# Performance work log

Hardware: AMD Instinct MI355X
Metric: run time of the kernel (lower is better)

## Reference

```python
import jax, jax.numpy as jnp
import numpy as np

VOCAB = 100000
DIM = 300
N, P, D = 4096, 10, 17  # samples, paths per sample (2C), padded path depth


def setup_inputs() -> dict:
    key = jax.random.key(0)
    k1, k2, k3, k4, k5 = jax.random.split(key, 5)
    word_idx = jax.random.randint(k1, (N,), 0, VOCAB)
    paths = jax.random.randint(k2, (N, P, D), 0, VOCAB - 1)   # inner-node ids
    labels = jax.random.randint(k3, (N, P, D), 0, 2)          # branch directions
    emb1 = jax.random.normal(k4, (VOCAB, DIM), dtype=jnp.float32) * 0.1
    emb2 = jax.random.normal(k5, (VOCAB - 1, DIM), dtype=jnp.float32) * 0.1
    return {"word_idx": word_idx, "paths": paths, "labels": labels,
            "emb1": emb1, "emb2": emb2}


def reference(word_idx, paths, labels, emb1, emb2):
    # proj = embedding_1(x_idx): [N, DIM]
    proj = emb1[word_idx]
    # hierarchy_vectors = embedding_2(dir_path): [N, P, D, DIM]
    hvecs = emb2[paths]
    # output = sigmoid(proj @ hvecs.T), batched over (N, P): [N, P, D]
    logits = jnp.einsum('nd,npkd->npk', proj, hvecs)
    output = jax.nn.sigmoid(logits)
    # mask[output >= 0.5] = 1; target[mask == label] = 1
    mask = (output >= 0.5).astype(labels.dtype)
    target = (mask == labels).astype(jnp.float32)
    return output, target
```

## Files before the change

### kernel.cpp

```cpp
#include <hip/hip_runtime.h>
#include <math.h>

#define NN 4096
#define PP 10
#define DD 17
#define DIM 300
#define NPD (NN * PP * DD)

__global__ __launch_bounds__(256) void hs_fwd_kernel(
    const int* __restrict__ word_idx,
    const int* __restrict__ paths,
    const int* __restrict__ labels,
    const float* __restrict__ emb1,
    const float* __restrict__ emb2,
    float* __restrict__ out,
    float* __restrict__ target)
{
    const int wave = (int)((blockIdx.x * blockDim.x + threadIdx.x) >> 6);
    const int lane = (int)(threadIdx.x & 63);
    if (wave >= NN * PP) return;
    const int n = wave / PP;
    const int j    = lane & 31;
    const int half = lane >> 5;

    const float4* p4 = (const float4*)(emb1 + (long long)word_idx[n] * DIM);
    const float4 pr0 = p4[j];
    const float4 pr1 = p4[j + 32];
    const float4 pr2 = (j < 11) ? p4[j + 64] : make_float4(0.f, 0.f, 0.f, 0.f);

    const long long base = (long long)wave * DD;
    const int my_path  = (lane < DD) ? paths[base + lane]  : 0;
    const int my_label = (lane < DD) ? labels[base + lane] : 0;

    float my_logit = 0.0f;

    #pragma unroll
    for (int i = 0; i < 9; ++i) {
        const int k = 2 * i + half;
        float acc = 0.0f;
        if (k < DD) {
            const int row = __shfl(my_path, k);
            const float4* r4 = (const float4*)(emb2 + (long long)row * DIM);
            const float4 a0 = r4[j];
            const float4 a1 = r4[j + 32];
            acc = pr0.x * a0.x + pr0.y * a0.y + pr0.z * a0.z + pr0.w * a0.w
                + pr1.x * a1.x + pr1.y * a1.y + pr1.z * a1.z + pr1.w * a1.w;
            if (j < 11) {
                const float4 a2 = r4[j + 64];
                acc += pr2.x * a2.x + pr2.y * a2.y + pr2.z * a2.z + pr2.w * a2.w;
            }
        }
        #pragma unroll
        for (int off = 16; off > 0; off >>= 1)
            acc += __shfl_xor(acc, off);
        const float other = __shfl_xor(acc, 32);
        if (lane == 2 * i) my_logit = acc;
        if (2 * i + 1 < DD && lane == 2 * i + 1) my_logit = other;
    }

    if (lane < DD) {
        const float o = 1.0f / (1.0f + expf(-my_logit));
        out[base + lane] = o;
        const int mask = (o >= 0.5f) ? 1 : 0;
        target[base + lane] = (mask == my_label) ? 1.0f : 0.0f;
    }
}

extern "C" void kernel_launch(void* const* d_in, const int* in_sizes, int n_in,
                              void* d_out, int out_size, void* d_ws, size_t ws_size,
                              hipStream_t stream) {
    const int*   word_idx = (const int*)d_in[0];
    const int*   paths    = (const int*)d_in[1];
    const int*   labels   = (const int*)d_in[2];
    const float* emb1     = (const float*)d_in[3];
    const float* emb2     = (const float*)d_in[4];

    float* out    = (float*)d_out;
    float* target = (float*)d_out + NPD;

    const int total_waves = NN * PP;
    const int waves_per_block = 4;
    const int blocks = (total_waves + waves_per_block - 1) / waves_per_block;

    hs_fwd_kernel<<<blocks, 256, 0, stream>>>(word_idx, paths, labels, emb1, emb2, out, target);
}
```

Baseline: 322.3 us.

## Counting-sort path entries by embedding row before gathering dot products

Builds a histogram, prefix scan and scatter that reorders all (sample, path, depth) entries by their emb2 row id. A per-entry kernel then processes them in row order, so repeated rows are read back-to-back and hit in cache instead of being gathered randomly. Entries whose logit is close to zero are queued and recomputed by the original per-path kernel, so the threshold decision keeps the original summation order. This adds several extra kernel launches, atomics, scattered output writes and workspace traffic in exchange for better emb2 locality.

```diff
diff --git a/kernel.cpp b/kernel.cpp
--- a/kernel.cpp
+++ b/kernel.cpp
@@ -7,7 +7,113 @@
 #define DIM 300
 #define NPD (NN * PP * DD)
 
-__global__ __launch_bounds__(256) void hs_fwd_kernel(
+#define T_ENT (NN * PP * DD)
+#define CNT_SZ 100352
+#define NB_SCAN 98
+#define REP_CAP 65536
+#define WS_NEEDED ((size_t)(CNT_SZ + 128 + 64 + T_ENT + REP_CAP) * 4)
+
+
+__global__ void k_zero(int* __restrict__ p, int n) {
+    int i = blockIdx.x * blockDim.x + threadIdx.x;
+    if (i < n) p[i] = 0;
+}
+
+__global__ void k_hist(const int* __restrict__ paths, int* __restrict__ cnt) {
+    int t = blockIdx.x * blockDim.x + threadIdx.x;
+    atomicAdd(&cnt[paths[t]], 1);
+}
+
+__global__ __launch_bounds__(1024) void k_scan1(int* __restrict__ cnt, int* __restrict__ bsum) {
+    __shared__ int s[1024];
+    const int tid = threadIdx.x;
+    const int i = blockIdx.x * 1024 + tid;
+    const int v = cnt[i];
+    s[tid] = v;
+    __syncthreads();
+    #pragma unroll
+    for (int off = 1; off < 1024; off <<= 1) {
+        int add = (tid >= off) ? s[tid - off] : 0;
+        __syncthreads();
+        s[tid] += add;
+        __syncthreads();
+    }
+    cnt[i] = s[tid] - v;
+    if (tid == 1023) bsum[blockIdx.x] = s[1023];
+}
+
+__global__ void k_scan2(int* __restrict__ bsum) {
+    if (threadIdx.x == 0) {
+        int acc = 0;
+        for (int b = 0; b < NB_SCAN; ++b) { int v = bsum[b]; bsum[b] = acc; acc += v; }
+    }
+}
+
+__global__ __launch_bounds__(1024) void k_scan3(int* __restrict__ cnt, const int* __restrict__ bsum) {
+    int i = blockIdx.x * 1024 + threadIdx.x;
+    cnt[i] += bsum[blockIdx.x];
+}
+
+__global__ void k_scatter(const int* __restrict__ paths, int* __restrict__ cursor,
+                          int* __restrict__ order) {
+    int t = blockIdx.x * blockDim.x + threadIdx.x;
+    int row = paths[t];
+    int pos = atomicAdd(&cursor[row], 1);
+    order[pos] = t;
+}
+
+__global__ __launch_bounds__(256) void k_proc(
+    const int* __restrict__ order,
+    const int* __restrict__ word_idx,
+    const int* __restrict__ paths,
+    const int* __restrict__ labels,
+    const float* __restrict__ emb1,
+    const float* __restrict__ emb2,
+    float* __restrict__ out,
+    float* __restrict__ target,
+    int* __restrict__ rep_cnt,
+    int* __restrict__ rep_list)
+{
+    const int per = gridDim.x >> 3;
+    const int vb  = (blockIdx.x & 7) * per + (blockIdx.x >> 3);
+    const int e = vb * 8 + (int)(threadIdx.x >> 5);
+    const int j = (int)(threadIdx.x & 31);
+    if (e >= T_ENT) return;
+
+    const int t   = order[e];
+    const int row = paths[t];
+    const int n   = t / (PP * DD);
+
+    const float4* p4 = (const float4*)(emb1 + (long long)word_idx[n] * DIM);
+    const float4* r4 = (const float4*)(emb2 + (long long)row * DIM);
+
+    const float4 p0 = p4[j],      r0 = r4[j];
+    const float4 p1 = p4[j + 32], r1 = r4[j + 32];
+    float acc = p0.x * r0.x + p0.y * r0.y + p0.z * r0.z + p0.w * r0.w
+              + p1.x * r1.x + p1.y * r1.y + p1.z * r1.z + p1.w * r1.w;
+    if (j < 11) {
+        const float4 p2 = p4[j + 64], r2 = r4[j + 64];
+        acc += p2.x * r2.x + p2.y * r2.y + p2.z * r2.z + p2.w * r2.w;
+    }
+    #pragma unroll
+    for (int off = 16; off > 0; off >>= 1)
+        acc += __shfl_xor(acc, off);
+
+    if (j == 0) {
+        const float o = 1.0f / (1.0f + expf(-acc));
+        out[t] = o;
+        const int mask = (o >= 0.5f) ? 1 : 0;
+        target[t] = (mask == labels[t]) ? 1.0f : 0.0f;
+        if (fabsf(acc) < 1e-4f) {
+            int pos = atomicAdd(rep_cnt, 1);
+            if (pos < REP_CAP) rep_list[pos] = t / DD;
+        }
+    }
+}
+
+__global__ __launch_bounds__(256) void k_repair(
+    const int* __restrict__ rep_cnt,
+    const int* __restrict__ rep_list,
     const int* __restrict__ word_idx,
     const int* __restrict__ paths,
     const int* __restrict__ labels,
@@ -16,11 +122,70 @@
     float* __restrict__ out,
     float* __restrict__ target)
 {
+    const int nrep = min(*rep_cnt, REP_CAP);
+    const int waves_per_grid = gridDim.x * (blockDim.x >> 6);
+    const int lane = (int)(threadIdx.x & 63);
+    for (int widx = blockIdx.x * (blockDim.x >> 6) + (int)(threadIdx.x >> 6);
+         widx < nrep; widx += waves_per_grid) {
+        const int wave = rep_list[widx];
+        if ((unsigned)wave >= (unsigned)(NN * PP)) continue;
+        const int n = wave / PP;
+        const int j    = lane & 31;
+        const int half = lane >> 5;
+
+        const float4* p4 = (const float4*)(emb1 + (long long)word_idx[n] * DIM);
+        const float4 pr0 = p4[j];
+        const float4 pr1 = p4[j + 32];
+        const float4 pr2 = (j < 11) ? p4[j + 64] : make_float4(0.f, 0.f, 0.f, 0.f);
+
+        const long long base = (long long)wave * DD;
+        const int my_path  = (lane < DD) ? paths[base + lane]  : 0;
+        const int my_label = (lane < DD) ? labels[base + lane] : 0;
+
+        float my_logit = 0.0f;
+        #pragma unroll
+        for (int i = 0; i < 9; ++i) {
+            const int k = 2 * i + half;
+            float acc = 0.0f;
+            if (k < DD) {
+                const int rrow = __shfl(my_path, k);
+                const float4* r4 = (const float4*)(emb2 + (long long)rrow * DIM);
+                const float4 a0 = r4[j];
+                const float4 a1 = r4[j + 32];
+                acc = pr0.x * a0.x + pr0.y * a0.y + pr0.z * a0.z + pr0.w * a0.w
+                    + pr1.x * a1.x + pr1.y * a1.y + pr1.z * a1.z + pr1.w * a1.w;
+                if (j < 11) {
+                    const float4 a2 = r4[j + 64];
+                    acc += pr2.x * a2.x + pr2.y * a2.y + pr2.z * a2.z + pr2.w * a2.w;
+                }
+            }
+            #pragma unroll
+            for (int off = 16; off > 0; off >>= 1)
+                acc += __shfl_xor(acc, off);
+            const float other = __shfl_xor(acc, 32);
+            if (lane == 2 * i) my_logit = acc;
+            if (2 * i + 1 < DD && lane == 2 * i + 1) my_logit = other;
+        }
+
+        if (lane < DD) {
+            const float o = 1.0f / (1.0f + expf(-my_logit));
+            out[base + lane] = o;
+            const int mask = (o >= 0.5f) ? 1 : 0;
+            target[base + lane] = (mask == my_label) ? 1.0f : 0.0f;
+        }
+    }
+}
+
+__global__ __launch_bounds__(256) void hs_fwd_kernel(
+    const int* __restrict__ word_idx, const int* __restrict__ paths,
+    const int* __restrict__ labels, const float* __restrict__ emb1,
+    const float* __restrict__ emb2, float* __restrict__ out, float* __restrict__ target)
+{
     const int wave = (int)((blockIdx.x * blockDim.x + threadIdx.x) >> 6);
     const int lane = (int)(threadIdx.x & 63);
     if (wave >= NN * PP) return;
     const int n = wave / PP;
-    const int j    = lane & 31;
+    const int j = lane & 31;
     const int half = lane >> 5;
 
     const float4* p4 = (const float4*)(emb1 + (long long)word_idx[n] * DIM);
@@ -33,7 +198,6 @@
     const int my_label = (lane < DD) ? labels[base + lane] : 0;
 
     float my_logit = 0.0f;
-
     #pragma unroll
     for (int i = 0; i < 9; ++i) {
         const int k = 2 * i + half;
@@ -78,9 +242,30 @@
     float* out    = (float*)d_out;
     float* target = (float*)d_out + NPD;
 
-    const int total_waves = NN * PP;
-    const int waves_per_block = 4;
-    const int blocks = (total_waves + waves_per_block - 1) / waves_per_block;
-
-    hs_fwd_kernel<<<blocks, 256, 0, stream>>>(word_idx, paths, labels, emb1, emb2, out, target);
-}
+    if (ws_size < WS_NEEDED || d_ws == nullptr) {
+        const int total_waves = NN * PP;
+        const int blocks = (total_waves * 64 + 255) / 256;
+        hs_fwd_kernel<<<blocks, 256, 0, stream>>>(word_idx, paths, labels, emb1, emb2, out, target);
+        return;
+    }
+
+    int* cursor   = (int*)d_ws;
+    int* bsum     = cursor + CNT_SZ;
+    int* rep_cnt  = bsum + 128;
+    int* order    = rep_cnt + 64;
+    int* rep_list = order + T_ENT;
+
+    {
+        const int n = CNT_SZ + 128 + 64;
+        k_zero<<<(n + 255) / 256, 256, 0, stream>>>(cursor, n);
+    }
+    k_hist<<<T_ENT / 256, 256, 0, stream>>>(paths, cursor);
+    k_scan1<<<NB_SCAN, 1024, 0, stream>>>(cursor, bsum);
+    k_scan2<<<1, 64, 0, stream>>>(bsum);
+    k_scan3<<<NB_SCAN, 1024, 0, stream>>>(cursor, bsum);
+    k_scatter<<<T_ENT / 256, 256, 0, stream>>>(paths, cursor, order);
+    k_proc<<<T_ENT / 8, 256, 0, stream>>>(order, word_idx, paths, labels,
+                                          emb1, emb2, out, target, rep_cnt, rep_list);
+    k_repair<<<64, 256, 0, stream>>>(rep_cnt, rep_list, word_idx, paths, labels,
+                                     emb1, emb2, out, target);
+}
```

After: 472.3 us. 1.47x slower.
